# Optimization experiments

Measured on AMD Instinct MI355X. Metric: run time of the kernel, lower is better.

## Reference

```python
import jax, jax.numpy as jnp
import numpy as np

B, N, H, NH = 8, 1024, 512, 8
DK = H // NH


def setup_inputs() -> dict:
    key = jax.random.key(0)
    ks = jax.random.split(key, 6)
    x = jax.random.normal(ks[0], (B, N, H), dtype=jnp.float32)
    adj = jax.random.randint(ks[1], (B, N, N), 0, 2, dtype=jnp.int32)
    # ensure no all-zero row (self-loops) so softmax is well-defined
    adj = jnp.maximum(adj, jnp.eye(N, dtype=jnp.int32)[None])
    s = 1.0 / np.sqrt(H)
    Wq = jax.random.normal(ks[2], (H, H), dtype=jnp.float32) * s
    Wk = jax.random.normal(ks[3], (H, H), dtype=jnp.float32) * s
    Wv = jax.random.normal(ks[4], (H, H), dtype=jnp.float32) * s
    Wg = jax.random.normal(ks[5], (H, 2 * H), dtype=jnp.float32) * (1.0 / np.sqrt(2 * H))
    bg = jnp.zeros((H,), dtype=jnp.float32)
    return {"x": x, "adj": adj, "Wq": Wq, "Wk": Wk, "Wv": Wv, "Wg": Wg, "bg": bg}


def reference(x, adj, Wq, Wk, Wv, Wg, bg):
    b, n, h = x.shape
    # projections (nn.Linear: x @ W.T), split heads -> [b, n, nh, dk]
    q = (x @ Wq.T).reshape(b, n, NH, DK)
    k = (x @ Wk.T).reshape(b, n, NH, DK)
    v = (x @ Wv.T).reshape(b, n, NH, DK)
    # scaled masked attention: [b, nh, n, n]
    scores = jnp.einsum('bqhd,bkhd->bhqk', q, k) / jnp.sqrt(jnp.float32(DK))
    mask = (adj != 0)[:, None, :, :]
    scores = jnp.where(mask, scores, -jnp.inf)
    attn = jax.nn.softmax(scores, axis=-1)  # dropout p=0.0 -> identity
    c = jnp.einsum('bhqk,bkhd->bqhd', attn, v).reshape(b, n, h)
    # sigmoid gated residual combine
    gate = jax.nn.sigmoid(jnp.concatenate([c, x], axis=2) @ Wg.T + bg)
    return gate * x + (1.0 - gate) * c
```

## Files before the change

### kernel.cpp

```cpp
#include <hip/hip_runtime.h>
#include <math.h>

#define B_  8
#define N_  1024
#define H_  512
#define NH_ 8
#define DK_ 64
#define M_  (B_ * N_)

typedef __attribute__((ext_vector_type(4))) float f32x4;
typedef __attribute__((ext_vector_type(8))) short bf16x8;

__device__ __forceinline__ unsigned short f2bf(float f) {
    unsigned int u = __float_as_uint(f);
    u = (u + 0x7fffu + ((u >> 16) & 1u)) >> 16;
    return (unsigned short)u;
}

__device__ __forceinline__ void gload16(const unsigned short* g, unsigned short* l) {
    __builtin_amdgcn_global_load_lds(
        (const __attribute__((address_space(1))) void*)g,
        (__attribute__((address_space(3))) void*)l, 16, 0, 0);
}

__global__ __launch_bounds__(256) void cvt_k(const float* __restrict__ src,
                                             unsigned short* __restrict__ dst, int n)
{
    int i = (blockIdx.x * 256 + threadIdx.x) * 4;
    if (i < n) {
        float4 v = *(const float4*)&src[i];
        *(ushort4*)&dst[i] = make_ushort4(f2bf(v.x), f2bf(v.y), f2bf(v.z), f2bf(v.w));
    }
}

__global__ __launch_bounds__(256) void pack_k(const int* __restrict__ adj,
                                              unsigned long long* __restrict__ mb)
{
    int gw   = (int)((blockIdx.x * 256 + threadIdx.x) >> 6);
    int lane = threadIdx.x & 63;
    int kt = gw & 15;
    int q  = (gw >> 4) & (N_ - 1);
    int b  = gw >> 14;
    int val = adj[(size_t)(b * N_ + q) * N_ + kt * 64 + lane];
    unsigned long long m = __ballot(val != 0);
    if (lane == 0) mb[gw] = m;
}

__global__ __launch_bounds__(256, 2) void proj_k(const unsigned short* __restrict__ xb,
                                                 const unsigned short* __restrict__ Wqb,
                                                 const unsigned short* __restrict__ Wkb,
                                                 const unsigned short* __restrict__ Wvb,
                                                 unsigned short* __restrict__ qkv)
{
    __shared__ unsigned short As[8192];
    __shared__ unsigned short Bs[8192];
    const int tid = threadIdx.x;
    const int lane = tid & 63, wv = tid >> 6;
    const int ln = lane & 15, quad = lane >> 4;
    const int wm = wv >> 1, wn = wv & 1;
    const int row0 = blockIdx.x * 128;
    const int w    = blockIdx.y >> 2;
    const int col0 = (blockIdx.y & 3) * 128;
    const unsigned short* W = (w == 0) ? Wqb : ((w == 1) ? Wkb : Wvb);
    f32x4 acc[4][4] = {};

    for (int kt = 0; kt < H_; kt += 64) {
        __syncthreads();
        #pragma unroll
        for (int i = 0; i < 4; ++i) {
            int c = tid + i * 256;
            int c8 = c >> 7, row = c & 127;
            gload16(&xb[(size_t)(row0 + row) * H_ + kt + c8 * 8], &As[c * 8]);
            gload16(&W [(size_t)(col0 + row) * H_ + kt + c8 * 8], &Bs[c * 8]);
        }
        __syncthreads();
        #pragma unroll
        for (int kk = 0; kk < 2; ++kk) {
            bf16x8 af[4], bf[4];
            #pragma unroll
            for (int t = 0; t < 4; ++t) {
                af[t] = *(const bf16x8*)&As[((kk * 4 + quad) * 128 + wm * 64 + t * 16 + ln) * 8];
                bf[t] = *(const bf16x8*)&Bs[((kk * 4 + quad) * 128 + wn * 64 + t * 16 + ln) * 8];
            }
            #pragma unroll
            for (int mt = 0; mt < 4; ++mt)
                #pragma unroll
                for (int nt = 0; nt < 4; ++nt)
                    acc[mt][nt] = __builtin_amdgcn_mfma_f32_16x16x32_bf16(af[mt], bf[nt], acc[mt][nt], 0, 0, 0);
        }
    }
    #pragma unroll
    for (int mt = 0; mt < 4; ++mt)
        #pragma unroll
        for (int nt = 0; nt < 4; ++nt)
            #pragma unroll
            for (int r = 0; r < 4; ++r) {
                int m = row0 + wm * 64 + mt * 16 + quad * 4 + r;
                int c = w * H_ + col0 + wn * 64 + nt * 16 + ln;
                qkv[(size_t)m * (3 * H_) + c] = f2bf(acc[mt][nt][r]);
            }
}

__global__ __launch_bounds__(256) void transp_k(const unsigned short* __restrict__ qkv,
                                                unsigned short* __restrict__ Vt)
{
    __shared__ unsigned short Ts[64][72];
    const int bh = blockIdx.x;
    const int n0 = blockIdx.y * 64;
    const int b = bh >> 3, h = bh & 7;
    const int tid = threadIdx.x;
    #pragma unroll
    for (int p = 0; p < 2; ++p) {
        int row = (tid >> 3) + p * 32;
        int ch  = tid & 7;
        *(uint4*)&Ts[row][ch * 8] =
            *(const uint4*)&qkv[(size_t)(b * N_ + n0 + row) * (3 * H_) + 2 * H_ + h * DK_ + ch * 8];
    }
    __syncthreads();
    #pragma unroll
    for (int p = 0; p < 16; ++p) {
        int d = (tid >> 6) + p * 4;
        int n = tid & 63;
        Vt[((size_t)bh * DK_ + d) * N_ + n0 + n] = Ts[n][d];
    }
}

__global__ __launch_bounds__(256, 4) void attn_k(const unsigned short* __restrict__ qkv,
                                                 const unsigned short* __restrict__ Vt,
                                                 const unsigned long long* __restrict__ Mb,
                                                 unsigned short* __restrict__ Cmb)
{
    const int nqt  = N_ / 64;
    const int qt   = blockIdx.x % nqt;
    const int head = (blockIdx.x / nqt) % NH_;
    const int b    = blockIdx.x / (nqt * NH_);

    __shared__ unsigned short Ks[4096];
    __shared__ unsigned short Vs[4096];
    __shared__ unsigned short Ps[4][16][72];

    const int tid = threadIdx.x;
    const int lane = tid & 63, wv = tid >> 6;
    const int ln = lane & 15, quad = lane >> 4;
    const int q = qt * 64 + wv * 16 + ln;

    bf16x8 bq[2];
    #pragma unroll
    for (int kk = 0; kk < 2; ++kk)
        bq[kk] = *(const bf16x8*)&qkv[(size_t)(b * N_ + q) * (3 * H_) + head * DK_ + kk * 32 + quad * 8];

    f32x4 o[4] = {};
    float psum = 0.f;
    const unsigned short* Kbase = qkv + H_ + head * DK_;

    for (int t = 0; t < 16; ++t) {
        const int kc = t * 64;
        __syncthreads();
        #pragma unroll
        for (int i = 0; i < 2; ++i) {
            int c = tid + i * 256;
            int c8 = c >> 6, row = c & 63;
            gload16(&Kbase[(size_t)(b * N_ + kc + row) * (3 * H_) + c8 * 8], &Ks[c * 8]);
            gload16(&Vt[((size_t)(b * NH_ + head) * DK_ + row) * N_ + kc + c8 * 8], &Vs[c * 8]);
        }
        __syncthreads();

        unsigned long long mq = Mb[(size_t)(b * N_ + q) * 16 + t];

        f32x4 s[4] = {};
        #pragma unroll
        for (int kk = 0; kk < 2; ++kk)
            #pragma unroll
            for (int nt = 0; nt < 4; ++nt) {
                bf16x8 ka = *(const bf16x8*)&Ks[((kk * 4 + quad) * 64 + nt * 16 + ln) * 8];
                s[nt] = __builtin_amdgcn_mfma_f32_16x16x32_bf16(ka, bq[kk], s[nt], 0, 0, 0);
            }

        unsigned long long sh = mq >> (quad * 4);
        #pragma unroll
        for (int nt = 0; nt < 4; ++nt) {
            unsigned int bn = (unsigned int)(sh >> (nt * 16)) & 0xFu;
            float p[4];
            #pragma unroll
            for (int r = 0; r < 4; ++r) {
                float e = __expf(s[nt][r] * 0.125f);
                p[r] = (bn & (1u << r)) ? e : 0.f;
                psum += p[r];
            }
            unsigned int d0 = __builtin_amdgcn_perm(__float_as_uint(p[1]), __float_as_uint(p[0]), 0x07060302u);
            unsigned int d1 = __builtin_amdgcn_perm(__float_as_uint(p[3]), __float_as_uint(p[2]), 0x07060302u);
            *(uint2*)&Ps[wv][ln][nt * 16 + quad * 4] = make_uint2(d0, d1);
        }

        bf16x8 pb[2];
        #pragma unroll
        for (int kk = 0; kk < 2; ++kk)
            pb[kk] = *(const bf16x8*)&Ps[wv][ln][kk * 32 + quad * 8];
        #pragma unroll
        for (int kk = 0; kk < 2; ++kk)
            #pragma unroll
            for (int dt = 0; dt < 4; ++dt) {
                bf16x8 va = *(const bf16x8*)&Vs[((kk * 4 + quad) * 64 + dt * 16 + ln) * 8];
                o[dt] = __builtin_amdgcn_mfma_f32_16x16x32_bf16(va, pb[kk], o[dt], 0, 0, 0);
            }
    }

    psum += __shfl_xor(psum, 16);
    psum += __shfl_xor(psum, 32);
    float inv = 1.f / psum;

    #pragma unroll
    for (int dt = 0; dt < 4; ++dt) {
        ushort4 u = make_ushort4(f2bf(o[dt][0] * inv), f2bf(o[dt][1] * inv),
                                 f2bf(o[dt][2] * inv), f2bf(o[dt][3] * inv));
        *(ushort4*)&Cmb[(size_t)(b * N_ + q) * H_ + head * DK_ + dt * 16 + quad * 4] = u;
    }
}

__global__ __launch_bounds__(256, 2) void gate_k(const unsigned short* __restrict__ cmb,
                                                 const unsigned short* __restrict__ xb,
                                                 const unsigned short* __restrict__ Wgb,
                                                 const float* __restrict__ bgp,
                                                 const float* __restrict__ X,
                                                 float* __restrict__ out)
{
    __shared__ unsigned short As[8192];
    __shared__ unsigned short Bs[4096];
    const int tid = threadIdx.x;
    const int lane = tid & 63, wv = tid >> 6;
    const int ln = lane & 15, quad = lane >> 4;
    const int wm = wv >> 1, wn = wv & 1;
    const int row0 = blockIdx.x * 128;
    const int col0 = blockIdx.y * 64;
    f32x4 acc[4][2] = {};

    for (int kt = 0; kt < 2 * H_; kt += 64) {
        const unsigned short* Asrc = (kt < H_) ? cmb : xb;
        const int ko = kt & (H_ - 1);
        __syncthreads();
        #pragma unroll
        for (int i = 0; i < 4; ++i) {
            int c = tid + i * 256;
            int c8 = c >> 7, row = c & 127;
            gload16(&Asrc[(size_t)(row0 + row) * H_ + ko + c8 * 8], &As[c * 8]);
        }
        #pragma unroll
        for (int i = 0; i < 2; ++i) {
            int c = tid + i * 256;
            int c8 = c >> 6, row = c & 63;
            gload16(&Wgb[(size_t)(col0 + row) * (2 * H_) + kt + c8 * 8], &Bs[c * 8]);
        }
        __syncthreads();
        #pragma unroll
        for (int kk = 0; kk < 2; ++kk) {
            bf16x8 af[4], bf[2];
            #pragma unroll
            for (int t = 0; t < 4; ++t)
                af[t] = *(const bf16x8*)&As[((kk * 4 + quad) * 128 + wm * 64 + t * 16 + ln) * 8];
            #pragma unroll
            for (int t = 0; t < 2; ++t)
                bf[t] = *(const bf16x8*)&Bs[((kk * 4 + quad) * 64 + wn * 32 + t * 16 + ln) * 8];
            #pragma unroll
            for (int mt = 0; mt < 4; ++mt)
                #pragma unroll
                for (int nt = 0; nt < 2; ++nt)
                    acc[mt][nt] = __builtin_amdgcn_mfma_f32_16x16x32_bf16(af[mt], bf[nt], acc[mt][nt], 0, 0, 0);
        }
    }
    #pragma unroll
    for (int mt = 0; mt < 4; ++mt)
        #pragma unroll
        for (int nt = 0; nt < 2; ++nt)
            #pragma unroll
            for (int r = 0; r < 4; ++r) {
                int m = row0 + wm * 64 + mt * 16 + quad * 4 + r;
                int c = col0 + wn * 32 + nt * 16 + ln;
                float g  = 1.f / (1.f + __expf(-(acc[mt][nt][r] + bgp[c])));
                float xv = X[(size_t)m * H_ + c];
                float cv = __uint_as_float(((unsigned int)cmb[(size_t)m * H_ + c]) << 16);
                out[(size_t)m * H_ + c] = g * xv + (1.f - g) * cv;
            }
}

extern "C" void kernel_launch(void* const* d_in, const int* in_sizes, int n_in,
                              void* d_out, int out_size, void* d_ws, size_t ws_size,
                              hipStream_t stream)
{
    const float* x   = (const float*)d_in[0];
    const int*   adj = (const int*)  d_in[1];
    const float* Wq  = (const float*)d_in[2];
    const float* Wk  = (const float*)d_in[3];
    const float* Wv  = (const float*)d_in[4];
    const float* Wg  = (const float*)d_in[5];
    const float* bg  = (const float*)d_in[6];
    float* out = (float*)d_out;

    unsigned short* xb  = (unsigned short*)d_ws;
    unsigned short* wqb = xb  + (size_t)M_ * H_;
    unsigned short* wkb = wqb + (size_t)H_ * H_;
    unsigned short* wvb = wkb + (size_t)H_ * H_;
    unsigned short* wgb = wvb + (size_t)H_ * H_;
    unsigned short* qkv = wgb + (size_t)H_ * 2 * H_;
    unsigned short* vt  = qkv + (size_t)M_ * 3 * H_;
    unsigned short* cmb = vt  + (size_t)M_ * H_;
    unsigned long long* mb = (unsigned long long*)(cmb + (size_t)M_ * H_);

    cvt_k<<<M_ * H_ / 1024, 256, 0, stream>>>(x, xb, M_ * H_);
    cvt_k<<<H_ * H_ / 1024, 256, 0, stream>>>(Wq, wqb, H_ * H_);
    cvt_k<<<H_ * H_ / 1024, 256, 0, stream>>>(Wk, wkb, H_ * H_);
    cvt_k<<<H_ * H_ / 1024, 256, 0, stream>>>(Wv, wvb, H_ * H_);
    cvt_k<<<H_ * 2 * H_ / 1024, 256, 0, stream>>>(Wg, wgb, H_ * 2 * H_);

    pack_k<<<M_ * 16 / 4, 256, 0, stream>>>(adj, mb);

    proj_k<<<dim3(M_ / 128, 12), 256, 0, stream>>>(xb, wqb, wkb, wvb, qkv);

    transp_k<<<dim3(B_ * NH_, N_ / 64), 256, 0, stream>>>(qkv, vt);

    attn_k<<<B_ * NH_ * (N_ / 64), 256, 0, stream>>>(qkv, vt, mb, cmb);

    gate_k<<<dim3(M_ / 128, H_ / 64), 256, 0, stream>>>(cmb, xb, wgb, bg, x, out);
}
```

Measured before the change: 234.5 us.

## Double-buffer attention K/V tiles, double queries per wave, fold scale into Wq

```diff
diff --git a/kernel.cpp b/kernel.cpp
--- a/kernel.cpp
+++ b/kernel.cpp
@@ -17,20 +17,42 @@
     return (unsigned short)u;
 }
 
+__device__ __forceinline__ float fexp2(float x) {
+#if __has_builtin(__builtin_amdgcn_exp2f)
+    return __builtin_amdgcn_exp2f(x);
+#else
+    return exp2f(x);
+#endif
+}
+
 __device__ __forceinline__ void gload16(const unsigned short* g, unsigned short* l) {
     __builtin_amdgcn_global_load_lds(
         (const __attribute__((address_space(1))) void*)g,
         (__attribute__((address_space(3))) void*)l, 16, 0, 0);
 }
 
-__global__ __launch_bounds__(256) void cvt_k(const float* __restrict__ src,
-                                             unsigned short* __restrict__ dst, int n)
-{
-    int i = (blockIdx.x * 256 + threadIdx.x) * 4;
-    if (i < n) {
-        float4 v = *(const float4*)&src[i];
-        *(ushort4*)&dst[i] = make_ushort4(f2bf(v.x), f2bf(v.y), f2bf(v.z), f2bf(v.w));
-    }
+__global__ __launch_bounds__(256) void cvt_all_k(const float* __restrict__ x,
+                                                 const float* __restrict__ Wq,
+                                                 const float* __restrict__ Wk,
+                                                 const float* __restrict__ Wv,
+                                                 const float* __restrict__ Wg,
+                                                 unsigned short* __restrict__ xb,
+                                                 unsigned short* __restrict__ wqb,
+                                                 unsigned short* __restrict__ wkb,
+                                                 unsigned short* __restrict__ wvb,
+                                                 unsigned short* __restrict__ wgb)
+{
+    int id = blockIdx.x;
+    const float* src; unsigned short* dst; int off; float scale = 1.0f;
+    if (id < 4096)      { src = x;  dst = xb;  off = id; }
+    else if (id < 4352) { src = Wq; dst = wqb; off = id - 4096; scale = 0.18033688011112042f; }
+    else if (id < 4608) { src = Wk; dst = wkb; off = id - 4352; }
+    else if (id < 4864) { src = Wv; dst = wvb; off = id - 4608; }
+    else                { src = Wg; dst = wgb; off = id - 4864; }
+    size_t i = (size_t)off * 1024 + threadIdx.x * 4;
+    float4 v = *(const float4*)&src[i];
+    *(ushort4*)&dst[i] = make_ushort4(f2bf(v.x * scale), f2bf(v.y * scale),
+                                      f2bf(v.z * scale), f2bf(v.w * scale));
 }
 
 __global__ __launch_bounds__(256) void pack_k(const int* __restrict__ adj,
@@ -46,7 +68,7 @@
     if (lane == 0) mb[gw] = m;
 }
 
-__global__ __launch_bounds__(256, 2) void proj_k(const unsigned short* __restrict__ xb,
+__global__ __launch_bounds__(256, 3) void proj_k(const unsigned short* __restrict__ xb,
                                                  const unsigned short* __restrict__ Wqb,
                                                  const unsigned short* __restrict__ Wkb,
                                                  const unsigned short* __restrict__ Wvb,
@@ -125,95 +147,119 @@
     }
 }
 
-__global__ __launch_bounds__(256, 4) void attn_k(const unsigned short* __restrict__ qkv,
+__global__ __launch_bounds__(256, 2) void attn_k(const unsigned short* __restrict__ qkv,
                                                  const unsigned short* __restrict__ Vt,
                                                  const unsigned long long* __restrict__ Mb,
                                                  unsigned short* __restrict__ Cmb)
 {
-    const int nqt  = N_ / 64;
+    const int nqt  = N_ / 128;
     const int qt   = blockIdx.x % nqt;
     const int head = (blockIdx.x / nqt) % NH_;
     const int b    = blockIdx.x / (nqt * NH_);
 
-    __shared__ unsigned short Ks[4096];
-    __shared__ unsigned short Vs[4096];
-    __shared__ unsigned short Ps[4][16][72];
+    __shared__ unsigned short Ks[2][4096];
+    __shared__ unsigned short Vs[2][4096];
+    __shared__ unsigned short Ps[4][2][16][72];
 
     const int tid = threadIdx.x;
     const int lane = tid & 63, wv = tid >> 6;
     const int ln = lane & 15, quad = lane >> 4;
-    const int q = qt * 64 + wv * 16 + ln;
-
-    bf16x8 bq[2];
-    #pragma unroll
-    for (int kk = 0; kk < 2; ++kk)
-        bq[kk] = *(const bf16x8*)&qkv[(size_t)(b * N_ + q) * (3 * H_) + head * DK_ + kk * 32 + quad * 8];
-
-    f32x4 o[4] = {};
-    float psum = 0.f;
+    const int q0 = qt * 128 + wv * 32 + ln;
+    const int q1 = q0 + 16;
+
     const unsigned short* Kbase = qkv + H_ + head * DK_;
-
-    for (int t = 0; t < 16; ++t) {
-        const int kc = t * 64;
-        __syncthreads();
+    const unsigned short* Vbase = Vt + (size_t)(b * NH_ + head) * DK_ * N_;
+
+    bf16x8 bq[2][2];
+    #pragma unroll
+    for (int kk = 0; kk < 2; ++kk) {
+        bq[0][kk] = *(const bf16x8*)&qkv[(size_t)(b * N_ + q0) * (3 * H_) + head * DK_ + kk * 32 + quad * 8];
+        bq[1][kk] = *(const bf16x8*)&qkv[(size_t)(b * N_ + q1) * (3 * H_) + head * DK_ + kk * 32 + quad * 8];
+    }
+
+    f32x4 o[2][4] = {};
+    float psum[2] = {0.f, 0.f};
+
+    auto issue = [&](int t, int bi) {
         #pragma unroll
         for (int i = 0; i < 2; ++i) {
             int c = tid + i * 256;
             int c8 = c >> 6, row = c & 63;
-            gload16(&Kbase[(size_t)(b * N_ + kc + row) * (3 * H_) + c8 * 8], &Ks[c * 8]);
-            gload16(&Vt[((size_t)(b * NH_ + head) * DK_ + row) * N_ + kc + c8 * 8], &Vs[c * 8]);
-        }
-        __syncthreads();
-
-        unsigned long long mq = Mb[(size_t)(b * N_ + q) * 16 + t];
-
-        f32x4 s[4] = {};
+            gload16(&Kbase[(size_t)(b * N_ + t * 64 + row) * (3 * H_) + c8 * 8], &Ks[bi][c * 8]);
+            gload16(&Vbase[(size_t)row * N_ + t * 64 + c8 * 8], &Vs[bi][c * 8]);
+        }
+    };
+
+    issue(0, 0);
+
+    for (int t = 0; t < 16; ++t) {
+        __syncthreads();
+        if (t < 15) issue(t + 1, (t + 1) & 1);
+        const unsigned short* Kc = Ks[t & 1];
+        const unsigned short* Vc = Vs[t & 1];
+
+        unsigned long long mq[2];
+        mq[0] = Mb[(size_t)(b * N_ + q0) * 16 + t];
+        mq[1] = Mb[(size_t)(b * N_ + q1) * 16 + t];
+
+        f32x4 s[2][4] = {};
         #pragma unroll
         for (int kk = 0; kk < 2; ++kk)
             #pragma unroll
             for (int nt = 0; nt < 4; ++nt) {
-                bf16x8 ka = *(const bf16x8*)&Ks[((kk * 4 + quad) * 64 + nt * 16 + ln) * 8];
-                s[nt] = __builtin_amdgcn_mfma_f32_16x16x32_bf16(ka, bq[kk], s[nt], 0, 0, 0);
-            }
-
-        unsigned long long sh = mq >> (quad * 4);
-        #pragma unroll
-        for (int nt = 0; nt < 4; ++nt) {
-            unsigned int bn = (unsigned int)(sh >> (nt * 16)) & 0xFu;
-            float p[4];
-            #pragma unroll
-            for (int r = 0; r < 4; ++r) {
-                float e = __expf(s[nt][r] * 0.125f);
-                p[r] = (bn & (1u << r)) ? e : 0.f;
-                psum += p[r];
-            }
-            unsigned int d0 = __builtin_amdgcn_perm(__float_as_uint(p[1]), __float_as_uint(p[0]), 0x07060302u);
-            unsigned int d1 = __builtin_amdgcn_perm(__float_as_uint(p[3]), __float_as_uint(p[2]), 0x07060302u);
-            *(uint2*)&Ps[wv][ln][nt * 16 + quad * 4] = make_uint2(d0, d1);
-        }
-
-        bf16x8 pb[2];
+                bf16x8 ka = *(const bf16x8*)&Kc[((kk * 4 + quad) * 64 + nt * 16 + ln) * 8];
+                s[0][nt] = __builtin_amdgcn_mfma_f32_16x16x32_bf16(ka, bq[0][kk], s[0][nt], 0, 0, 0);
+                s[1][nt] = __builtin_amdgcn_mfma_f32_16x16x32_bf16(ka, bq[1][kk], s[1][nt], 0, 0, 0);
+            }
+
+        #pragma unroll
+        for (int g = 0; g < 2; ++g) {
+            unsigned long long sh = mq[g] >> (quad * 4);
+            #pragma unroll
+            for (int nt = 0; nt < 4; ++nt) {
+                unsigned int bn = (unsigned int)(sh >> (nt * 16)) & 0xFu;
+                float p[4];
+                #pragma unroll
+                for (int r = 0; r < 4; ++r) {
+                    float e = fexp2(s[g][nt][r]);
+                    p[r] = (bn & (1u << r)) ? e : 0.f;
+                    psum[g] += p[r];
+                }
+                unsigned int d0 = __builtin_amdgcn_perm(__float_as_uint(p[1]), __float_as_uint(p[0]), 0x07060302u);
+                unsigned int d1 = __builtin_amdgcn_perm(__float_as_uint(p[3]), __float_as_uint(p[2]), 0x07060302u);
+                *(uint2*)&Ps[wv][g][ln][nt * 16 + quad * 4] = make_uint2(d0, d1);
+            }
+        }
+
+        bf16x8 pb[2][2];
+        #pragma unroll
+        for (int g = 0; g < 2; ++g)
+            #pragma unroll
+            for (int kk = 0; kk < 2; ++kk)
+                pb[g][kk] = *(const bf16x8*)&Ps[wv][g][ln][kk * 32 + quad * 8];
+
         #pragma unroll
         for (int kk = 0; kk < 2; ++kk)
-            pb[kk] = *(const bf16x8*)&Ps[wv][ln][kk * 32 + quad * 8];
-        #pragma unroll
-        for (int kk = 0; kk < 2; ++kk)
             #pragma unroll
             for (int dt = 0; dt < 4; ++dt) {
-                bf16x8 va = *(const bf16x8*)&Vs[((kk * 4 + quad) * 64 + dt * 16 + ln) * 8];
-                o[dt] = __builtin_amdgcn_mfma_f32_16x16x32_bf16(va, pb[kk], o[dt], 0, 0, 0);
-            }
-    }
-
-    psum += __shfl_xor(psum, 16);
-    psum += __shfl_xor(psum, 32);
-    float inv = 1.f / psum;
-
-    #pragma unroll
-    for (int dt = 0; dt < 4; ++dt) {
-        ushort4 u = make_ushort4(f2bf(o[dt][0] * inv), f2bf(o[dt][1] * inv),
-                                 f2bf(o[dt][2] * inv), f2bf(o[dt][3] * inv));
-        *(ushort4*)&Cmb[(size_t)(b * N_ + q) * H_ + head * DK_ + dt * 16 + quad * 4] = u;
+                bf16x8 va = *(const bf16x8*)&Vc[((kk * 4 + quad) * 64 + dt * 16 + ln) * 8];
+                o[0][dt] = __builtin_amdgcn_mfma_f32_16x16x32_bf16(va, pb[0][kk], o[0][dt], 0, 0, 0);
+                o[1][dt] = __builtin_amdgcn_mfma_f32_16x16x32_bf16(va, pb[1][kk], o[1][dt], 0, 0, 0);
+            }
+    }
+
+    #pragma unroll
+    for (int g = 0; g < 2; ++g) {
+        psum[g] += __shfl_xor(psum[g], 16);
+        psum[g] += __shfl_xor(psum[g], 32);
+        float inv = 1.f / psum[g];
+        int qg = (g == 0) ? q0 : q1;
+        #pragma unroll
+        for (int dt = 0; dt < 4; ++dt) {
+            ushort4 u = make_ushort4(f2bf(o[g][dt][0] * inv), f2bf(o[g][dt][1] * inv),
+                                     f2bf(o[g][dt][2] * inv), f2bf(o[g][dt][3] * inv));
+            *(ushort4*)&Cmb[(size_t)(b * N_ + qg) * H_ + head * DK_ + dt * 16 + quad * 4] = u;
+        }
     }
 }
 
@@ -305,11 +351,7 @@
     unsigned short* cmb = vt  + (size_t)M_ * H_;
     unsigned long long* mb = (unsigned long long*)(cmb + (size_t)M_ * H_);
 
-    cvt_k<<<M_ * H_ / 1024, 256, 0, stream>>>(x, xb, M_ * H_);
-    cvt_k<<<H_ * H_ / 1024, 256, 0, stream>>>(Wq, wqb, H_ * H_);
-    cvt_k<<<H_ * H_ / 1024, 256, 0, stream>>>(Wk, wkb, H_ * H_);
-    cvt_k<<<H_ * H_ / 1024, 256, 0, stream>>>(Wv, wvb, H_ * H_);
-    cvt_k<<<H_ * 2 * H_ / 1024, 256, 0, stream>>>(Wg, wgb, H_ * 2 * H_);
+    cvt_all_k<<<5376, 256, 0, stream>>>(x, Wq, Wk, Wv, Wg, xb, wqb, wkb, wvb, wgb);
 
     pack_k<<<M_ * 16 / 4, 256, 0, stream>>>(adj, mb);
 
@@ -317,7 +359,7 @@
 
     transp_k<<<dim3(B_ * NH_, N_ / 64), 256, 0, stream>>>(qkv, vt);
 
-    attn_k<<<B_ * NH_ * (N_ / 64), 256, 0, stream>>>(qkv, vt, mb, cmb);
+    attn_k<<<B_ * NH_ * (N_ / 128), 256, 0, stream>>>(qkv, vt, mb, cmb);
 
     gate_k<<<dim3(M_ / 128, H_ / 64), 256, 0, stream>>>(cmb, xb, wgb, bg, x, out);
 }
```

New measurement: 218.3 us. -6.9%, faster.
